# Performance work log

Measured on AMD Instinct MI355X. Metric: run time of the kernel, lower is better.

The kernel has to match this reference:

```python
import jax, jax.numpy as jnp
import numpy as np


def setup_inputs() -> dict:
    key = jax.random.key(0)
    k1, k2, k3, k4, k5 = jax.random.split(key, 5)
    B, F, E, NF = 16384, 1024, 64, 32
    return {
        "input": jax.random.normal(k1, (B, F), dtype=jnp.float32),
        "fields": jax.random.randint(k2, (F,), 0, NF, dtype=jnp.int32),
        "w_weight": jax.random.normal(k3, (1, F), dtype=jnp.float32) * 0.02,
        "w_bias": jax.random.normal(k4, (1,), dtype=jnp.float32) * 0.02,
        "vs": jax.random.normal(k5, (NF, F, E), dtype=jnp.float32) * 0.05,
    }


def reference(input, fields, w_weight, w_bias, vs):
    # Linear (1st-order) term: [B, 1]
    linear = input @ w_weight.T + w_bias

    F = input.shape[1]
    # Gather field-aware embedding tables per feature: G[k, i, e] = vs[fields[k], i, e]
    G = vs[fields]  # [F, F, E]
    # A[i, j] = dot(vs[fields[j], i, :], vs[fields[i], j, :])
    A = jnp.einsum("jie,ije->ij", G, G)  # [F, F]
    # P[i, j] = sum_b input[b, i] * input[b, j]  (original sums over batch)
    P = input.T @ input  # [F, F]
    # second_order = sum_{i < j} A[i, j] * P[i, j]  (scalar, as in the source)
    second_order = jnp.sum(jnp.triu(A * P, k=1))

    return jax.nn.sigmoid(linear + second_order)
```

## Files before the change

kernel.cpp:

```cpp
#include <hip/hip_runtime.h>
#include <hip/hip_fp16.h>
#include <math.h>
#include <stdint.h>

#define FDIM 1024
#define BTOT 16384
#define EDIM 64
#define NFLD 32
#define NPANEL 4
#define NPAIRS 10

typedef _Float16 half8 __attribute__((ext_vector_type(8)));
typedef float f32x4 __attribute__((ext_vector_type(4)));

__device__ __forceinline__ uint32_t pkh(float a, float b){
  _Float16 lo = (_Float16)a, hi = (_Float16)b;
  uint16_t ulo = __builtin_bit_cast(uint16_t, lo);
  uint16_t uhi = __builtin_bit_cast(uint16_t, hi);
  return ((uint32_t)uhi << 16) | (uint32_t)ulo;
}

__device__ __forceinline__ void gload16(const void* g, void* l){
  __builtin_amdgcn_global_load_lds((const __attribute__((address_space(1))) void*)g,
                                   (__attribute__((address_space(3))) void*)l,
                                   16, 0, 0);
}

__device__ __forceinline__ float fget(const float4& v, int i){
  switch (i){ case 0: return v.x; case 1: return v.y; case 2: return v.z; default: return v.w; }
}

__device__ __forceinline__ int pairId(int ti, int tj){
  return ti * NPANEL - (ti * (ti + 1)) / 2 + tj;
}

__global__ __launch_bounds__(256) void mid_fused(
    const float* __restrict__ vs, const int* __restrict__ fields,
    _Float16* __restrict__ Wp,
    const float* __restrict__ X, const float* __restrict__ w,
    uint4* __restrict__ Xbt, float* __restrict__ linp){
  const int t = threadIdx.x;

  if (blockIdx.x >= 1024){
    __shared__ uint4 tb[4][256];
    const int bx = blockIdx.x - 1024;
    const int p  = bx & 3;
    const int kb = bx >> 2;
    const int ro = t >> 6;
    const int l  = t & 63;
    const int og = kb * 4 + ro;
    const int k0 = og * 8;
    const int c0 = p * 256;

    float4 rv[8];
#pragma unroll
    for (int r = 0; r < 8; ++r)
      rv[r] = *(const float4*)(X + (size_t)(k0 + r) * FDIM + c0 + l * 4);

    const float4 w4 = *(const float4*)(w + c0 + l * 4);
#pragma unroll
    for (int r = 0; r < 8; ++r){
      float lp = rv[r].x * w4.x + rv[r].y * w4.y + rv[r].z * w4.z + rv[r].w * w4.w;
#pragma unroll
      for (int off = 32; off; off >>= 1) lp += __shfl_xor(lp, off, 64);
      if (l == 0) linp[(size_t)p * BTOT + k0 + r] = lp;
    }

#pragma unroll
    for (int i = 0; i < 4; ++i){
      uint4 ch;
      ch.x = pkh(fget(rv[0], i), fget(rv[1], i));
      ch.y = pkh(fget(rv[2], i), fget(rv[3], i));
      ch.z = pkh(fget(rv[4], i), fget(rv[5], i));
      ch.w = pkh(fget(rv[6], i), fget(rv[7], i));
      tb[ro][l * 4 + i] = ch;
    }
    __syncthreads();
    uint4* dst = Xbt + ((size_t)p * 2048 + og) * 256;
#pragma unroll
    for (int i = 0; i < 4; ++i)
      dst[l + 64 * i] = tb[ro][l + 64 * i];
    return;
  }

  __shared__ float Si[64][68];
  __shared__ float Sj[64][68];
  __shared__ int gI[64], gJ[64];
  __shared__ int cnt[NFLD], pos[NFLD], off[NFLD + 1];
  __shared__ int permS[FDIM];

  if (t < NFLD) cnt[t] = 0;
  __syncthreads();
#pragma unroll
  for (int r = 0; r < 4; ++r) atomicAdd(&cnt[fields[t + 256 * r]], 1);
  __syncthreads();
  if (t == 0){
    int s = 0;
    for (int i = 0; i < NFLD; ++i){ off[i] = s; s += cnt[i]; }
    off[NFLD] = s;
  }
  __syncthreads();
  if (t < NFLD) pos[t] = off[t];
  __syncthreads();
#pragma unroll
  for (int r = 0; r < 4; ++r){
    const int idx = t + 256 * r;
    const int p = atomicAdd(&pos[fields[idx]], 1);
    permS[p] = idx;
  }
  __syncthreads();

  const int a = blockIdx.x >> 5, b = blockIdx.x & 31;
  const int oa = off[a], na = off[a + 1] - oa;
  const int ob = off[b], nb_ = off[b + 1] - ob;
  if (na == 0 || nb_ == 0) return;
  for (int ia0 = 0; ia0 < na; ia0 += 64){
    const int nac = min(64, na - ia0);
    for (int jb0 = 0; jb0 < nb_; jb0 += 64){
      const int nbc = min(64, nb_ - jb0);
      __syncthreads();
      if (t < 64){
        gI[t] = (t < nac) ? permS[oa + ia0 + t] : 0;
        gJ[t] = (t < nbc) ? permS[ob + jb0 + t] : 0;
      }
      __syncthreads();
#pragma unroll
      for (int rep = 0; rep < 4; ++rep){
        const int lidx = rep * 256 + t;
        const int r = lidx >> 4, e4 = (lidx & 15) * 4;
        if (r < nac)
          *(float4*)&Si[r][e4] = *(const float4*)(vs + ((size_t)b * FDIM + gI[r]) * EDIM + e4);
        if (r < nbc)
          *(float4*)&Sj[r][e4] = *(const float4*)(vs + ((size_t)a * FDIM + gJ[r]) * EDIM + e4);
      }
      __syncthreads();
      const int jr = t & 63;
      for (int ko = 0; ko * 4 < nac; ++ko){
        const int ir = ko * 4 + (t >> 6);
        if (ir < nac && jr < nbc){
          float dot = 0.f;
#pragma unroll
          for (int e4 = 0; e4 < EDIM; e4 += 4){
            const float4 x = *(const float4*)&Si[ir][e4];
            const float4 y = *(const float4*)&Sj[jr][e4];
            dot += x.x * y.x + x.y * y.y + x.z * y.z + x.w * y.w;
          }
          const int gi = gI[ir], gj = gJ[jr];
          const int pi = gi >> 8, pj = gj >> 8;
          if (pi <= pj){
            const float v = (gj > gi) ? dot : 0.f;
            const int li = gi & 255, lj = gj & 255;
            const int P  = pairId(pi, pj);
            const int w8 = (li >> 7) * 4 + (lj >> 6);
            const int mb = (li >> 4) & 7, r_ = li & 3;
            const int lane = ((li >> 2) & 3) * 16 + (lj & 15);
            const int nbv = (lj >> 4) & 3;
            const size_t o_ = (size_t)(P * 8 + w8) * 8192
                            + (size_t)((mb * 2 + (r_ >> 1)) * 64 + lane) * 8
                            + (r_ & 1) * 4 + nbv;
            Wp[o_] = (_Float16)v;
          }
        }
      }
    }
  }
}

__global__ __launch_bounds__(512, 2) void gram_kc(
    const uint4* __restrict__ Xbt, const _Float16* __restrict__ Wp,
    float* __restrict__ partial){
  __shared__ uint4 lds4[8192];
  const int t = threadIdx.x, w = t >> 6, lane = t & 63;
  const int orow = lane >> 4, rl = lane & 15;
  const int wr = w >> 2, wc = w & 3;
  const int b8 = blockIdx.x * 8;

#pragma unroll
  for (int p = 0; p < NPANEL; ++p)
#pragma unroll
    for (int q = 0; q < 4; ++q){
      const int m = q * 512 + t;
      const int o = m >> 8, c = m & 255;
      gload16(Xbt + ((size_t)p * 2048 + b8 + o) * 256 + c,
              lds4 + o * 1024 + p * 256 + c);
    }

  float wsum = 0.f;

  auto loadB = [&](int tj, half8 (&bf)[2][4]){
#pragma unroll
    for (int s = 0; s < 2; ++s)
#pragma unroll
      for (int nb = 0; nb < 4; ++nb)
        bf[s][nb] = __builtin_bit_cast(half8,
            lds4[(s * 4 + orow) * 1024 + tj * 256 + wc * 64 + nb * 16 + rl]);
  };

  auto body = [&](int ti, int tj, const half8 (&bf)[2][4]){
    f32x4 acc[8][4];
#pragma unroll
    for (int i = 0; i < 8; ++i)
#pragma unroll
      for (int j = 0; j < 4; ++j) acc[i][j] = {0.f, 0.f, 0.f, 0.f};
#pragma unroll
    for (int s = 0; s < 2; ++s)
#pragma unroll
      for (int mb = 0; mb < 8; ++mb){
        const half8 af = __builtin_bit_cast(half8,
            lds4[(s * 4 + orow) * 1024 + ti * 256 + wr * 128 + mb * 16 + rl]);
#pragma unroll
        for (int nb = 0; nb < 4; ++nb)
          acc[mb][nb] = __builtin_amdgcn_mfma_f32_16x16x32_f16(
              af, bf[s][nb], acc[mb][nb], 0, 0, 0);
      }
    const uint4* wp = (const uint4*)(Wp + (size_t)(pairId(ti, tj) * 8 + w) * 8192);
#pragma unroll
    for (int mb = 0; mb < 8; ++mb)
#pragma unroll
      for (int h = 0; h < 2; ++h){
        const half8 hv = __builtin_bit_cast(half8, wp[(mb * 2 + h) * 64 + lane]);
#pragma unroll
        for (int r2 = 0; r2 < 2; ++r2)
#pragma unroll
          for (int nb = 0; nb < 4; ++nb)
            wsum += (float)hv[r2 * 4 + nb] * acc[mb][nb][2 * h + r2];
      }
  };

#define GRAM_GROUP(G, VM)                                         \
  asm volatile("s_waitcnt vmcnt(" #VM ")" ::: "memory");          \
  __builtin_amdgcn_s_barrier();                                   \
  {                                                               \
    half8 bf[2][4];                                               \
    loadB(G, bf);                                                 \
    _Pragma("unroll 1")                                           \
    for (int ti = 0; ti <= (G); ++ti) body(ti, (G), bf);          \
  }

  GRAM_GROUP(0, 12)
  GRAM_GROUP(1, 8)
  GRAM_GROUP(2, 4)
  GRAM_GROUP(3, 0)
#undef GRAM_GROUP

#pragma unroll
  for (int off = 32; off; off >>= 1) wsum += __shfl_xor(wsum, off, 64);
  __syncthreads();
  float* red = (float*)lds4;
  if (lane == 0) red[w] = wsum;
  __syncthreads();
  if (t == 0){
    float s = 0.f;
#pragma unroll
    for (int i = 0; i < 8; ++i) s += red[i];
    partial[blockIdx.x] = s;
  }
}

__global__ __launch_bounds__(256) void final_out(
    const float* __restrict__ partial, const float* __restrict__ linp,
    const float* __restrict__ wb, float* __restrict__ out){
  __shared__ float red[256];
  const int t = threadIdx.x;
  red[t] = partial[t];
  __syncthreads();
  for (int off = 128; off; off >>= 1){
    if (t < off) red[t] += red[t + off];
    __syncthreads();
  }
  const float stot = red[0] + wb[0];
  const int i = blockIdx.x * 256 + t;
  float z = stot;
#pragma unroll
  for (int p = 0; p < NPANEL; ++p) z += linp[(size_t)p * BTOT + i];
  out[i] = 1.f / (1.f + expf(-z));
}

extern "C" void kernel_launch(void* const* d_in, const int* in_sizes, int n_in,
                              void* d_out, int out_size, void* d_ws,
                              size_t ws_size, hipStream_t stream) {
  const float* X      = (const float*)d_in[0];
  const int* fields   = (const int*)d_in[1];
  const float* ww     = (const float*)d_in[2];
  const float* wbias  = (const float*)d_in[3];
  const float* vs     = (const float*)d_in[4];
  float* out          = (float*)d_out;

  char* ws = (char*)d_ws;
  float* partial = (float*)ws;
  float* linp = (float*)(ws + (64 << 10));
  _Float16* Wp = (_Float16*)(ws + (size_t)(4 << 20));
  uint4* Xbt = (uint4*)(ws + (size_t)(8 << 20));


  mid_fused<<<1024 + 2048, 256, 0, stream>>>(vs, fields, Wp, X, ww, Xbt, linp);
  gram_kc<<<256, 512, 0, stream>>>(Xbt, Wp, partial);
  final_out<<<BTOT / 256, 256, 0, stream>>>(partial, linp, wbias, out);
}
```

Baseline: 70.07 us.

## Drop LDS transpose in X pack, shrink pair tiles, reorder blocks

```diff
diff --git a/kernel.cpp b/kernel.cpp
--- a/kernel.cpp
+++ b/kernel.cpp
@@ -11,13 +11,12 @@
 #define NPAIRS 10
 
 typedef _Float16 half8 __attribute__((ext_vector_type(8)));
+typedef __fp16 fp16x2 __attribute__((ext_vector_type(2)));
 typedef float f32x4 __attribute__((ext_vector_type(4)));
 
-__device__ __forceinline__ uint32_t pkh(float a, float b){
-  _Float16 lo = (_Float16)a, hi = (_Float16)b;
-  uint16_t ulo = __builtin_bit_cast(uint16_t, lo);
-  uint16_t uhi = __builtin_bit_cast(uint16_t, hi);
-  return ((uint32_t)uhi << 16) | (uint32_t)ulo;
+__device__ __forceinline__ uint32_t pk2(float a, float b){
+  fp16x2 h = __builtin_amdgcn_cvt_pkrtz(a, b);
+  return __builtin_bit_cast(uint32_t, h);
 }
 
 __device__ __forceinline__ void gload16(const void* g, void* l){
@@ -26,24 +25,19 @@
                                    16, 0, 0);
 }
 
-__device__ __forceinline__ float fget(const float4& v, int i){
-  switch (i){ case 0: return v.x; case 1: return v.y; case 2: return v.z; default: return v.w; }
-}
-
 __device__ __forceinline__ int pairId(int ti, int tj){
   return ti * NPANEL - (ti * (ti + 1)) / 2 + tj;
 }
 
-__global__ __launch_bounds__(256) void mid_fused(
+__global__ __launch_bounds__(256, 6) void mid_fused(
     const float* __restrict__ vs, const int* __restrict__ fields,
     _Float16* __restrict__ Wp,
     const float* __restrict__ X, const float* __restrict__ w,
     uint4* __restrict__ Xbt, float* __restrict__ linp){
   const int t = threadIdx.x;
 
-  if (blockIdx.x >= 1024){
-    __shared__ uint4 tb[4][256];
-    const int bx = blockIdx.x - 1024;
+  if (blockIdx.x < 2048){
+    const int bx = blockIdx.x;
     const int p  = bx & 3;
     const int kb = bx >> 2;
     const int ro = t >> 6;
@@ -52,40 +46,41 @@
     const int k0 = og * 8;
     const int c0 = p * 256;
 
-    float4 rv[8];
+    float xs[8][4];
 #pragma unroll
     for (int r = 0; r < 8; ++r)
-      rv[r] = *(const float4*)(X + (size_t)(k0 + r) * FDIM + c0 + l * 4);
-
-    const float4 w4 = *(const float4*)(w + c0 + l * 4);
+#pragma unroll
+      for (int i = 0; i < 4; ++i)
+        xs[r][i] = X[(size_t)(k0 + r) * FDIM + c0 + i * 64 + l];
+
+    float wv[4];
+#pragma unroll
+    for (int i = 0; i < 4; ++i) wv[i] = w[c0 + i * 64 + l];
 #pragma unroll
     for (int r = 0; r < 8; ++r){
-      float lp = rv[r].x * w4.x + rv[r].y * w4.y + rv[r].z * w4.z + rv[r].w * w4.w;
+      float lp = xs[r][0] * wv[0] + xs[r][1] * wv[1]
+               + xs[r][2] * wv[2] + xs[r][3] * wv[3];
 #pragma unroll
       for (int off = 32; off; off >>= 1) lp += __shfl_xor(lp, off, 64);
       if (l == 0) linp[(size_t)p * BTOT + k0 + r] = lp;
     }
 
+    uint4* dst = Xbt + ((size_t)p * 2048 + og) * 256;
 #pragma unroll
     for (int i = 0; i < 4; ++i){
       uint4 ch;
-      ch.x = pkh(fget(rv[0], i), fget(rv[1], i));
-      ch.y = pkh(fget(rv[2], i), fget(rv[3], i));
-      ch.z = pkh(fget(rv[4], i), fget(rv[5], i));
-      ch.w = pkh(fget(rv[6], i), fget(rv[7], i));
-      tb[ro][l * 4 + i] = ch;
-    }
-    __syncthreads();
-    uint4* dst = Xbt + ((size_t)p * 2048 + og) * 256;
-#pragma unroll
-    for (int i = 0; i < 4; ++i)
-      dst[l + 64 * i] = tb[ro][l + 64 * i];
+      ch.x = pk2(xs[0][i], xs[1][i]);
+      ch.y = pk2(xs[2][i], xs[3][i]);
+      ch.z = pk2(xs[4][i], xs[5][i]);
+      ch.w = pk2(xs[6][i], xs[7][i]);
+      dst[l + 64 * i] = ch;
+    }
     return;
   }
 
-  __shared__ float Si[64][68];
-  __shared__ float Sj[64][68];
-  __shared__ int gI[64], gJ[64];
+  __shared__ float Si[32][68];
+  __shared__ float Sj[32][68];
+  __shared__ int gI[32], gJ[32];
   __shared__ int cnt[NFLD], pos[NFLD], off[NFLD + 1];
   __shared__ int permS[FDIM];
 
@@ -110,22 +105,22 @@
   }
   __syncthreads();
 
-  const int a = blockIdx.x >> 5, b = blockIdx.x & 31;
+  const int a = (blockIdx.x - 2048) >> 5, b = (blockIdx.x - 2048) & 31;
   const int oa = off[a], na = off[a + 1] - oa;
   const int ob = off[b], nb_ = off[b + 1] - ob;
   if (na == 0 || nb_ == 0) return;
-  for (int ia0 = 0; ia0 < na; ia0 += 64){
-    const int nac = min(64, na - ia0);
-    for (int jb0 = 0; jb0 < nb_; jb0 += 64){
-      const int nbc = min(64, nb_ - jb0);
+  for (int ia0 = 0; ia0 < na; ia0 += 32){
+    const int nac = min(32, na - ia0);
+    for (int jb0 = 0; jb0 < nb_; jb0 += 32){
+      const int nbc = min(32, nb_ - jb0);
       __syncthreads();
-      if (t < 64){
+      if (t < 32){
         gI[t] = (t < nac) ? permS[oa + ia0 + t] : 0;
         gJ[t] = (t < nbc) ? permS[ob + jb0 + t] : 0;
       }
       __syncthreads();
 #pragma unroll
-      for (int rep = 0; rep < 4; ++rep){
+      for (int rep = 0; rep < 2; ++rep){
         const int lidx = rep * 256 + t;
         const int r = lidx >> 4, e4 = (lidx & 15) * 4;
         if (r < nac)
@@ -134,9 +129,10 @@
           *(float4*)&Sj[r][e4] = *(const float4*)(vs + ((size_t)a * FDIM + gJ[r]) * EDIM + e4);
       }
       __syncthreads();
-      const int jr = t & 63;
-      for (int ko = 0; ko * 4 < nac; ++ko){
-        const int ir = ko * 4 + (t >> 6);
+      const int jr = t & 31;
+      const int ir0 = t >> 5;
+      for (int ko = 0; ko * 8 < nac; ++ko){
+        const int ir = ko * 8 + ir0;
         if (ir < nac && jr < nbc){
           float dot = 0.f;
 #pragma unroll
@@ -293,7 +289,7 @@
   uint4* Xbt = (uint4*)(ws + (size_t)(8 << 20));
 
 
-  mid_fused<<<1024 + 2048, 256, 0, stream>>>(vs, fields, Wp, X, ww, Xbt, linp);
+  mid_fused<<<2048 + 1024, 256, 0, stream>>>(vs, fields, Wp, X, ww, Xbt, linp);
   gram_kc<<<256, 512, 0, stream>>>(Xbt, Wp, partial);
   final_out<<<BTOT / 256, 256, 0, stream>>>(partial, linp, wbias, out);
 }
```

Result: faster. 67.84 us (-3.2%).
